# Kernel tuning notes

Measured on AMD Instinct MI355X. Metric: run time of the kernel, lower is better.

Reference implementation:

```python
import jax, jax.numpy as jnp
import numpy as np

SIZE = 2048
N_TASKS = 8
REDUCTION = 16
HID = SIZE // REDUCTION  # 128
B = 4096
INIT_STD = 0.01


def setup_inputs() -> dict:
    key = jax.random.key(0)
    k1, k2, k3 = jax.random.split(key, 3)
    x = jax.random.normal(k1, (B, SIZE), dtype=jnp.float32)
    task_id = jax.random.randint(k2, (B,), 0, N_TASKS, dtype=jnp.int64)
    kd, ku = jax.random.split(k3)
    # torch Linear weight is [out, in]; store transposed [in, out] per task
    Wd = jax.random.normal(kd, (N_TASKS, SIZE, HID), dtype=jnp.float32) * INIT_STD
    bd = jnp.zeros((N_TASKS, HID), dtype=jnp.float32)
    Wu = jax.random.normal(ku, (N_TASKS, HID, SIZE), dtype=jnp.float32) * INIT_STD
    bu = jnp.zeros((N_TASKS, SIZE), dtype=jnp.float32)
    return {"x": x, "Wd": Wd, "bd": bd, "Wu": Wu, "bu": bu, "task_id": task_id}


def reference(x, Wd, bd, Wu, bu, task_id):
    # residual=True (default). Compute every expert's adapter output densely
    # (T small), then combine per-sample by task_id; task_id == -1 -> passthrough.
    h = jax.nn.silu(jnp.einsum('bd,tdh->bth', x, Wd) + bd[None])        # [B,T,HID]
    out_all = jnp.einsum('bth,thd->btd', h, Wu) + bu[None]              # [B,T,SIZE]
    tid = jnp.clip(task_id, 0, N_TASKS - 1)
    out_sel = jnp.take_along_axis(out_all, tid[:, None, None], axis=1)[:, 0]  # [B,SIZE]
    valid = (task_id >= 0)[:, None]
    return jnp.where(valid, x + out_sel, x)
```

## Files before the change

kernel.cpp:

```cpp
#include <hip/hip_runtime.h>

#define BN 4096
#define SZ 2048
#define HIDN 128
#define NT 8
#define PADROWS 4384
#define PADTILES (PADROWS / 16)

typedef __bf16 bf16_t;
typedef bf16_t bf16x4 __attribute__((ext_vector_type(4)));
typedef bf16_t bf16x8 __attribute__((ext_vector_type(8)));
typedef float f32x4 __attribute__((ext_vector_type(4)));

__device__ inline bf16_t f2b(float f) {
    unsigned u = __builtin_bit_cast(unsigned, f);
    unsigned short s = (unsigned short)((u + 0x7fffu + ((u >> 16) & 1u)) >> 16);
    return __builtin_bit_cast(bf16_t, s);
}


__device__ inline int detect_i64(const int* task, int tid, int* sflag) {
    if (tid < 64) {
        int v = task[2 * tid + 1];
        bool ok = (v == 0 || v == -1);
        unsigned long long m = __ballot(ok);
        if (tid == 0) *sflag = (m == ~0ull) ? 1 : 0;
    }
    return 0;
}

__global__ __launch_bounds__(256) void k_prep(const float* __restrict__ Wd,
                                              const int* __restrict__ task,
                                              bf16_t* __restrict__ WdP,
                                              int* __restrict__ cnt16g) {
    int bid = blockIdx.x, tid = threadIdx.x;
    __shared__ int wv[4][9], sflag;
    if (bid >= 512) {
        int blk = bid - 512;
        int lane = tid & 63, w = tid >> 6;
        detect_i64(task, tid, &sflag);
        __syncthreads();
        int f = sflag;
        int item = blk * 256 + tid;
        int tv = f ? task[2 * item] : task[item];
        int bk = (tv < 0) ? 8 : (tv > 7 ? 7 : tv);
#pragma unroll
        for (int bu = 0; bu < 9; bu++) {
            unsigned long long m = __ballot(bk == bu);
            if (lane == 0) wv[w][bu] = (int)__popcll(m);
        }
        __syncthreads();
        if (tid < 9) {
            int s = 0;
#pragma unroll
            for (int ww = 0; ww < 4; ww++) s += wv[ww][tid];
            cnt16g[blk * 9 + tid] = s;
        }
        return;
    }
    __shared__ float tile[32][132];
    int t = bid >> 6, kt = bid & 63;
    const float* src = Wd + ((size_t)t * SZ + kt * 32) * HIDN;
    bf16_t* dst = WdP + ((size_t)(t * 8) * 64 + kt) * 512;
#pragma unroll
    for (int i = 0; i < 4; i++) {
        int row = (tid >> 5) + 8 * i, quad = tid & 31;
        f32x4 v = *(const f32x4*)(src + (size_t)row * HIDN + quad * 4);
        tile[row][quad * 4 + 0] = v.x; tile[row][quad * 4 + 1] = v.y;
        tile[row][quad * 4 + 2] = v.z; tile[row][quad * 4 + 3] = v.w;
    }
    __syncthreads();
    int w = tid >> 6, lane = tid & 63, lr = lane & 15, lq = lane >> 4;
#pragma unroll
    for (int ii = 0; ii < 2; ii++) {
        int hf = w * 2 + ii;
        bf16x8 o;
#pragma unroll
        for (int j = 0; j < 8; j++) {
            int kloc = (j < 4) ? (4 * lq + j) : (16 + 4 * lq + j - 4);
            o[j] = f2b(tile[kloc][hf * 16 + lr]);
        }
        *(bf16x8*)(dst + (size_t)hf * 64 * 512 + lane * 8) = o;
    }
}

__global__ __launch_bounds__(256) void k_scatter(const int* __restrict__ task,
                                                 const int* __restrict__ cnt16g,
                                                 int* __restrict__ meta,
                                                 int* __restrict__ idxb) {
    __shared__ int c16s[16][9], tot[9], pre9[9], off[10], wv[4][9], sflag;
    int tid = threadIdx.x, lane = tid & 63, w = tid >> 6, blk = blockIdx.x;
    detect_i64(task, tid, &sflag);
    if (tid < 144) ((int*)c16s)[tid] = cnt16g[tid];
    __syncthreads();
    int f = sflag;
    int item = blk * 256 + tid;
    int tv = f ? task[2 * item] : task[item];
    int bk = (tv < 0) ? 8 : (tv > 7 ? 7 : tv);
    unsigned long long mymask = 0;
#pragma unroll
    for (int bu = 0; bu < 9; bu++) {
        unsigned long long m = __ballot(bk == bu);
        if (lane == 0) wv[w][bu] = (int)__popcll(m);
        if (bk == bu) mymask = m;
    }
    int rank = (int)__popcll(mymask & ((1ull << lane) - 1ull));
    __syncthreads();
    if (tid < 9) {
        int t = 0;
#pragma unroll
        for (int b = 0; b < 16; b++) t += c16s[b][tid];
        tot[tid] = t;
        int p = 0;
        for (int b = 0; b < blk; b++) p += c16s[b][tid];
        pre9[tid] = p;
        int s = 0;
#pragma unroll
        for (int ww = 0; ww < 4; ww++) { int q = wv[ww][tid]; wv[ww][tid] = s; s += q; }
    }
    __syncthreads();
    if (tid == 0) {
        int s = 0;
        for (int i = 0; i < 9; i++) { off[i] = s; s += (tot[i] + 31) & ~31; }
        off[9] = s;
    }
    __syncthreads();
    int pos = off[bk] + pre9[bk] + wv[w][bk] + rank;
    idxb[pos] = item;
    if (blk == 0) {
        if (tid < 9) meta[tid] = tot[tid];
        if (tid >= 16 && tid < 26) meta[tid] = off[tid - 16];
    }
}

__global__ __launch_bounds__(256) void k_gemm1(const float* __restrict__ x,
                                               const float* __restrict__ Wu,
                                               const bf16_t* __restrict__ WdP,
                                               bf16_t* __restrict__ WuP,
                                               const float* __restrict__ bd,
                                               const int* __restrict__ idxb,
                                               const int* __restrict__ meta,
                                               bf16_t* __restrict__ HbP) {
    int bid = blockIdx.x;
    int tid = threadIdx.x, lane = tid & 63, w = tid >> 6;
    int lr = lane & 15, lq = lane >> 4;
    if (bid >= 4096) {
        __shared__ float tile[32][132];
        int lb = bid - 4096;
        int t = lb >> 6, rem = lb & 63;
        int kf = rem >> 4, cch = rem & 15;
        const float* src = Wu + ((size_t)t * HIDN + kf * 32) * SZ + cch * 128;
        bf16_t* dst = WuP + ((size_t)(t * 128 + cch * 8) * 4 + kf) * 512;
#pragma unroll
        for (int i = 0; i < 4; i++) {
            int row = (tid >> 5) + 8 * i, quad = tid & 31;
            f32x4 v = *(const f32x4*)(src + (size_t)row * SZ + quad * 4);
            tile[row][quad * 4 + 0] = v.x; tile[row][quad * 4 + 1] = v.y;
            tile[row][quad * 4 + 2] = v.z; tile[row][quad * 4 + 3] = v.w;
        }
        __syncthreads();
#pragma unroll
        for (int ii = 0; ii < 2; ii++) {
            int hf = w * 2 + ii;
            bf16x8 o;
#pragma unroll
            for (int j = 0; j < 8; j++) {
                int kloc = (j < 4) ? (4 * lq + j) : (16 + 4 * lq + j - 4);
                o[j] = f2b(tile[kloc][hf * 16 + lr]);
            }
            *(bf16x8*)(dst + (size_t)hf * 4 * 512 + lane * 8) = o;
        }
        return;
    }
    int t = bid & 7, hh = (bid >> 3) & 1, tile = bid >> 4;
    int n = meta[t];
    int r0 = tile * 16;
    if (r0 >= n) return;
    int base = meta[16 + t];

    __shared__ int sg[16];
    __shared__ bf16_t xl[2][16][260];
    __shared__ bf16_t hl[16][68];
    if (tid < 16) {
        int r = r0 + tid;
        sg[tid] = idxb[base + (r < n ? r : n - 1)];
    }
    __syncthreads();

    f32x4 pre[4];
#pragma unroll
    for (int rr = 0; rr < 4; rr++)
        pre[rr] = *(const f32x4*)(x + (size_t)sg[w * 4 + rr] * SZ + lane * 4);
#pragma unroll
    for (int rr = 0; rr < 4; rr++) {
        bf16x4 v = {f2b(pre[rr].x), f2b(pre[rr].y), f2b(pre[rr].z), f2b(pre[rr].w)};
        *(bf16x4*)(&xl[0][w * 4 + rr][lane * 4]) = v;
    }
    __syncthreads();

    const bf16_t* wb = WdP + ((size_t)(t * 8 + hh * 4 + w) * 64) * 512 + lane * 8;
    f32x4 acc = {};
    for (int c = 0; c < 8; c++) {
        int cur = c & 1;
        if (c < 7) {
#pragma unroll
            for (int rr = 0; rr < 4; rr++)
                pre[rr] = *(const f32x4*)(x + (size_t)sg[w * 4 + rr] * SZ +
                                          (c + 1) * 256 + lane * 4);
        }
#pragma unroll
        for (int k8 = 0; k8 < 8; k8++) {
            int kf = c * 8 + k8;
            bf16x4 alo = *(const bf16x4*)(&xl[cur][lr][k8 * 32 + 4 * lq]);
            bf16x4 ahi = *(const bf16x4*)(&xl[cur][lr][k8 * 32 + 16 + 4 * lq]);
            bf16x8 a;
            a[0] = alo[0]; a[1] = alo[1]; a[2] = alo[2]; a[3] = alo[3];
            a[4] = ahi[0]; a[5] = ahi[1]; a[6] = ahi[2]; a[7] = ahi[3];
            bf16x8 b = *(const bf16x8*)(wb + (size_t)kf * 512);
            acc = __builtin_amdgcn_mfma_f32_16x16x32_bf16(a, b, acc, 0, 0, 0);
        }
        if (c < 7) {
#pragma unroll
            for (int rr = 0; rr < 4; rr++) {
                bf16x4 v = {f2b(pre[rr].x), f2b(pre[rr].y), f2b(pre[rr].z), f2b(pre[rr].w)};
                *(bf16x4*)(&xl[cur ^ 1][w * 4 + rr][lane * 4]) = v;
            }
        }
        __syncthreads();
    }

    {
        float bb = bd[t * HIDN + hh * 64 + w * 16 + lr];
#pragma unroll
        for (int reg = 0; reg < 4; reg++) {
            float v = acc[reg] + bb;
            hl[4 * lq + reg][w * 16 + lr] = f2b(v / (1.f + __expf(-v)));
        }
    }
    __syncthreads();
    if (w < 2) {
        int rt = (base + r0) >> 4;
        bf16x8 o;
#pragma unroll
        for (int j = 0; j < 8; j++) {
            int k = w * 32 + ((j < 4) ? (4 * lq + j) : (16 + 4 * lq + j - 4));
            o[j] = hl[lr][k];
        }
        *(bf16x8*)(HbP + ((size_t)(rt * 4 + hh * 2 + w) * 64 + lane) * 8) = o;
    }
}

__global__ __launch_bounds__(256) void k_gemm2(const float* __restrict__ x,
                                               const bf16_t* __restrict__ WuP,
                                               const float* __restrict__ bu,
                                               const bf16_t* __restrict__ HbP,
                                               const int* __restrict__ idxb,
                                               const int* __restrict__ meta,
                                               float* __restrict__ out) {
    int bid = blockIdx.x;
    int tid = threadIdx.x;
    if (bid >= 16384) {
        int pb = bid - 16384;
        int n8 = meta[8];
        int tile = pb & 127, half = pb >> 7;
        int r0 = tile * 32;
        if (r0 >= n8) return;
        int base8 = meta[16 + 8];
        int row = tid >> 3, cq = tid & 7;
        int r = r0 + row;
        if (r < n8) {
            int g = idxb[base8 + r];
            const f32x4* xs = (const f32x4*)(x + (size_t)g * SZ + half * 256) + cq;
            f32x4* os = (f32x4*)(out + (size_t)g * SZ + half * 256) + cq;
#pragma unroll
            for (int j = 0; j < 8; j++) __builtin_nontemporal_store(xs[j * 8], &os[j * 8]);
        }
        return;
    }
    int t = bid & 7, tile = (bid >> 3) & 127, cchunk = bid >> 10;
    int n = meta[t];
    int r0 = tile * 32;
    if (r0 >= n) return;
    int base = meta[16 + t];
    int lane = tid & 63, w = tid >> 6;
    int wr = w & 1, wc = w >> 1, lr = lane & 15, lq = lane >> 4;

    int rt = (base + r0) / 16 + wr;
    const bf16_t* ap = HbP + (size_t)rt * 4 * 512 + lane * 8;
    bf16x8 a[4];
#pragma unroll
    for (int kf = 0; kf < 4; kf++) a[kf] = *(const bf16x8*)(ap + kf * 512);

    const bf16_t* bp = WuP + ((size_t)(t * 128 + cchunk * 8 + wc * 4) * 4) * 512 + lane * 8;
    f32x4 acc[4] = {};
#pragma unroll
    for (int cf = 0; cf < 4; cf++) {
#pragma unroll
        for (int kf = 0; kf < 4; kf++) {
            bf16x8 b = *(const bf16x8*)(bp + (size_t)(cf * 4 + kf) * 512);
            acc[cf] = __builtin_amdgcn_mfma_f32_16x16x32_bf16(a[kf], b, acc[cf], 0, 0, 0);
        }
    }

    int gr[4];
#pragma unroll
    for (int reg = 0; reg < 4; reg++) {
        int r = r0 + wr * 16 + 4 * lq + reg;
        gr[reg] = (r < n) ? idxb[base + r] : -1;
    }
#pragma unroll
    for (int cf = 0; cf < 4; cf++) {
        int c = cchunk * 128 + wc * 64 + cf * 16 + lr;
        float bb = bu[t * SZ + c];
#pragma unroll
        for (int reg = 0; reg < 4; reg++) {
            if (gr[reg] >= 0) {
                size_t o = (size_t)gr[reg] * SZ + c;
                __builtin_nontemporal_store(x[o] + acc[cf][reg] + bb, &out[o]);
            }
        }
    }
}

extern "C" void kernel_launch(void* const* d_in, const int* in_sizes, int n_in,
                              void* d_out, int out_size, void* d_ws, size_t ws_size,
                              hipStream_t stream) {
    const float* x  = (const float*)d_in[0];
    const float* Wd = (const float*)d_in[1];
    const float* bd = (const float*)d_in[2];
    const float* Wu = (const float*)d_in[3];
    const float* bu = (const float*)d_in[4];
    const int* task = (const int*)d_in[5];
    float* out = (float*)d_out;

    char* ws = (char*)d_ws;
    int* idxb    = (int*)ws;
    int* meta    = (int*)(ws + 17664);
    int* cnt16   = (int*)(ws + 17920);
    bf16_t* HbP  = (bf16_t*)(ws + 18560);
    bf16_t* WdP  = (bf16_t*)(ws + 1140864);
    bf16_t* WuP  = (bf16_t*)(ws + 5335168);

    k_prep<<<528, 256, 0, stream>>>(Wd, task, WdP, cnt16);
    k_scatter<<<16, 256, 0, stream>>>(task, cnt16, meta, idxb);
    k_gemm1<<<4096 + 512, 256, 0, stream>>>(x, Wu, WdP, WuP, bd, idxb, meta, HbP);
    k_gemm2<<<16384 + 1024, 256, 0, stream>>>(x, WuP, bu, HbP, idxb, meta, out);
}
```

Measured before the change: 48.73 us.

## Reschedule weight packing: tiny histogram kernel, pack both weights alongside scatter

The histogram now runs as its own small 16-block kernel. The Wd and Wu fp32-to-bf16 packing blocks move into a single kernel that also performs the index scatter. Before, Wd packing ran with the histogram and Wu packing ran as extra blocks inside gemm1. This shortens the first dependent kernel and takes the packing tail off the gemm1 grid, but the scatter now waits behind a kernel that holds all of the weight conversion work.

```diff
diff --git a/kernel.cpp b/kernel.cpp
--- a/kernel.cpp
+++ b/kernel.cpp
@@ -29,43 +29,109 @@
     return 0;
 }
 
-__global__ __launch_bounds__(256) void k_prep(const float* __restrict__ Wd,
-                                              const int* __restrict__ task,
-                                              bf16_t* __restrict__ WdP,
+__global__ __launch_bounds__(256) void k_hist(const int* __restrict__ task,
                                               int* __restrict__ cnt16g) {
+    __shared__ int wv[4][9], sflag;
+    int tid = threadIdx.x, blk = blockIdx.x;
+    int lane = tid & 63, w = tid >> 6;
+    detect_i64(task, tid, &sflag);
+    __syncthreads();
+    int f = sflag;
+    int item = blk * 256 + tid;
+    int tv = f ? task[2 * item] : task[item];
+    int bk = (tv < 0) ? 8 : (tv > 7 ? 7 : tv);
+#pragma unroll
+    for (int bu = 0; bu < 9; bu++) {
+        unsigned long long m = __ballot(bk == bu);
+        if (lane == 0) wv[w][bu] = (int)__popcll(m);
+    }
+    __syncthreads();
+    if (tid < 9) {
+        int s = 0;
+#pragma unroll
+        for (int ww = 0; ww < 4; ww++) s += wv[ww][tid];
+        cnt16g[blk * 9 + tid] = s;
+    }
+}
+
+__global__ __launch_bounds__(256) void k_pack_scatter(const float* __restrict__ Wd,
+                                                      const float* __restrict__ Wu,
+                                                      const int* __restrict__ task,
+                                                      const int* __restrict__ cnt16g,
+                                                      bf16_t* __restrict__ WdP,
+                                                      bf16_t* __restrict__ WuP,
+                                                      int* __restrict__ meta,
+                                                      int* __restrict__ idxb) {
     int bid = blockIdx.x, tid = threadIdx.x;
-    __shared__ int wv[4][9], sflag;
-    if (bid >= 512) {
-        int blk = bid - 512;
-        int lane = tid & 63, w = tid >> 6;
+    if (bid < 16) {
+        __shared__ int c16s[16][9], tot[9], pre9[9], off[10], wv[4][9], sflag;
+        int lane = tid & 63, w = tid >> 6, blk = bid;
         detect_i64(task, tid, &sflag);
+        if (tid < 144) ((int*)c16s)[tid] = cnt16g[tid];
         __syncthreads();
         int f = sflag;
         int item = blk * 256 + tid;
         int tv = f ? task[2 * item] : task[item];
         int bk = (tv < 0) ? 8 : (tv > 7 ? 7 : tv);
+        unsigned long long mymask = 0;
 #pragma unroll
         for (int bu = 0; bu < 9; bu++) {
             unsigned long long m = __ballot(bk == bu);
             if (lane == 0) wv[w][bu] = (int)__popcll(m);
-        }
+            if (bk == bu) mymask = m;
+        }
+        int rank = (int)__popcll(mymask & ((1ull << lane) - 1ull));
         __syncthreads();
         if (tid < 9) {
+            int t = 0;
+#pragma unroll
+            for (int b = 0; b < 16; b++) t += c16s[b][tid];
+            tot[tid] = t;
+            int p = 0;
+            for (int b = 0; b < blk; b++) p += c16s[b][tid];
+            pre9[tid] = p;
             int s = 0;
 #pragma unroll
-            for (int ww = 0; ww < 4; ww++) s += wv[ww][tid];
-            cnt16g[blk * 9 + tid] = s;
+            for (int ww = 0; ww < 4; ww++) { int q = wv[ww][tid]; wv[ww][tid] = s; s += q; }
+        }
+        __syncthreads();
+        if (tid == 0) {
+            int s = 0;
+            for (int i = 0; i < 9; i++) { off[i] = s; s += (tot[i] + 31) & ~31; }
+            off[9] = s;
+        }
+        __syncthreads();
+        idxb[off[bk] + pre9[bk] + wv[w][bk] + rank] = item;
+        if (blk == 0) {
+            if (tid < 9) meta[tid] = tot[tid];
+            if (tid >= 16 && tid < 26) meta[tid] = off[tid - 16];
         }
         return;
     }
     __shared__ float tile[32][132];
-    int t = bid >> 6, kt = bid & 63;
-    const float* src = Wd + ((size_t)t * SZ + kt * 32) * HIDN;
-    bf16_t* dst = WdP + ((size_t)(t * 8) * 64 + kt) * 512;
+    const float* src;
+    bf16_t* dst;
+    int fragstride;
+    size_t rowstride;
+    if (bid < 528) {
+        int lb = bid - 16;
+        int t = lb >> 6, kt = lb & 63;
+        src = Wd + ((size_t)t * SZ + kt * 32) * HIDN;
+        rowstride = HIDN;
+        dst = WdP + ((size_t)(t * 8) * 64 + kt) * 512;
+        fragstride = 64 * 512;
+    } else {
+        int lb = bid - 528;
+        int t = lb >> 6, rem = lb & 63, kf = rem >> 4, cch = rem & 15;
+        src = Wu + ((size_t)t * HIDN + kf * 32) * SZ + cch * 128;
+        rowstride = SZ;
+        dst = WuP + ((size_t)(t * 128 + cch * 8) * 4 + kf) * 512;
+        fragstride = 4 * 512;
+    }
 #pragma unroll
     for (int i = 0; i < 4; i++) {
         int row = (tid >> 5) + 8 * i, quad = tid & 31;
-        f32x4 v = *(const f32x4*)(src + (size_t)row * HIDN + quad * 4);
+        f32x4 v = *(const f32x4*)(src + (size_t)row * rowstride + quad * 4);
         tile[row][quad * 4 + 0] = v.x; tile[row][quad * 4 + 1] = v.y;
         tile[row][quad * 4 + 2] = v.z; tile[row][quad * 4 + 3] = v.w;
     }
@@ -80,63 +146,12 @@
             int kloc = (j < 4) ? (4 * lq + j) : (16 + 4 * lq + j - 4);
             o[j] = f2b(tile[kloc][hf * 16 + lr]);
         }
-        *(bf16x8*)(dst + (size_t)hf * 64 * 512 + lane * 8) = o;
-    }
-}
-
-__global__ __launch_bounds__(256) void k_scatter(const int* __restrict__ task,
-                                                 const int* __restrict__ cnt16g,
-                                                 int* __restrict__ meta,
-                                                 int* __restrict__ idxb) {
-    __shared__ int c16s[16][9], tot[9], pre9[9], off[10], wv[4][9], sflag;
-    int tid = threadIdx.x, lane = tid & 63, w = tid >> 6, blk = blockIdx.x;
-    detect_i64(task, tid, &sflag);
-    if (tid < 144) ((int*)c16s)[tid] = cnt16g[tid];
-    __syncthreads();
-    int f = sflag;
-    int item = blk * 256 + tid;
-    int tv = f ? task[2 * item] : task[item];
-    int bk = (tv < 0) ? 8 : (tv > 7 ? 7 : tv);
-    unsigned long long mymask = 0;
-#pragma unroll
-    for (int bu = 0; bu < 9; bu++) {
-        unsigned long long m = __ballot(bk == bu);
-        if (lane == 0) wv[w][bu] = (int)__popcll(m);
-        if (bk == bu) mymask = m;
-    }
-    int rank = (int)__popcll(mymask & ((1ull << lane) - 1ull));
-    __syncthreads();
-    if (tid < 9) {
-        int t = 0;
-#pragma unroll
-        for (int b = 0; b < 16; b++) t += c16s[b][tid];
-        tot[tid] = t;
-        int p = 0;
-        for (int b = 0; b < blk; b++) p += c16s[b][tid];
-        pre9[tid] = p;
-        int s = 0;
-#pragma unroll
-        for (int ww = 0; ww < 4; ww++) { int q = wv[ww][tid]; wv[ww][tid] = s; s += q; }
-    }
-    __syncthreads();
-    if (tid == 0) {
-        int s = 0;
-        for (int i = 0; i < 9; i++) { off[i] = s; s += (tot[i] + 31) & ~31; }
-        off[9] = s;
-    }
-    __syncthreads();
-    int pos = off[bk] + pre9[bk] + wv[w][bk] + rank;
-    idxb[pos] = item;
-    if (blk == 0) {
-        if (tid < 9) meta[tid] = tot[tid];
-        if (tid >= 16 && tid < 26) meta[tid] = off[tid - 16];
+        *(bf16x8*)(dst + (size_t)hf * fragstride + lane * 8) = o;
     }
 }
 
 __global__ __launch_bounds__(256) void k_gemm1(const float* __restrict__ x,
-                                               const float* __restrict__ Wu,
                                                const bf16_t* __restrict__ WdP,
-                                               bf16_t* __restrict__ WuP,
                                                const float* __restrict__ bd,
                                                const int* __restrict__ idxb,
                                                const int* __restrict__ meta,
@@ -144,34 +159,6 @@
     int bid = blockIdx.x;
     int tid = threadIdx.x, lane = tid & 63, w = tid >> 6;
     int lr = lane & 15, lq = lane >> 4;
-    if (bid >= 4096) {
-        __shared__ float tile[32][132];
-        int lb = bid - 4096;
-        int t = lb >> 6, rem = lb & 63;
-        int kf = rem >> 4, cch = rem & 15;
-        const float* src = Wu + ((size_t)t * HIDN + kf * 32) * SZ + cch * 128;
-        bf16_t* dst = WuP + ((size_t)(t * 128 + cch * 8) * 4 + kf) * 512;
-#pragma unroll
-        for (int i = 0; i < 4; i++) {
-            int row = (tid >> 5) + 8 * i, quad = tid & 31;
-            f32x4 v = *(const f32x4*)(src + (size_t)row * SZ + quad * 4);
-            tile[row][quad * 4 + 0] = v.x; tile[row][quad * 4 + 1] = v.y;
-            tile[row][quad * 4 + 2] = v.z; tile[row][quad * 4 + 3] = v.w;
-        }
-        __syncthreads();
-#pragma unroll
-        for (int ii = 0; ii < 2; ii++) {
-            int hf = w * 2 + ii;
-            bf16x8 o;
-#pragma unroll
-            for (int j = 0; j < 8; j++) {
-                int kloc = (j < 4) ? (4 * lq + j) : (16 + 4 * lq + j - 4);
-                o[j] = f2b(tile[kloc][hf * 16 + lr]);
-            }
-            *(bf16x8*)(dst + (size_t)hf * 4 * 512 + lane * 8) = o;
-        }
-        return;
-    }
     int t = bid & 7, hh = (bid >> 3) & 1, tile = bid >> 4;
     int n = meta[t];
     int r0 = tile * 16;
@@ -341,8 +328,8 @@
     bf16_t* WdP  = (bf16_t*)(ws + 1140864);
     bf16_t* WuP  = (bf16_t*)(ws + 5335168);
 
-    k_prep<<<528, 256, 0, stream>>>(Wd, task, WdP, cnt16);
-    k_scatter<<<16, 256, 0, stream>>>(task, cnt16, meta, idxb);
-    k_gemm1<<<4096 + 512, 256, 0, stream>>>(x, Wu, WdP, WuP, bd, idxb, meta, HbP);
+    k_hist<<<16, 256, 0, stream>>>(task, cnt16);
+    k_pack_scatter<<<1040, 256, 0, stream>>>(Wd, Wu, task, cnt16, WdP, WuP, meta, idxb);
+    k_gemm1<<<4096, 256, 0, stream>>>(x, WdP, bd, idxb, meta, HbP);
     k_gemm2<<<16384 + 1024, 256, 0, stream>>>(x, WuP, bu, HbP, idxb, meta, out);
 }
```

New measurement: 50.36 us. 1.03x slower.
